# Kernel optimization log

Measured on AMD Instinct MI355X. Metric: run time of the kernel, lower is better.

The kernel has to match this reference:

```python
import jax, jax.numpy as jnp
import numpy as np

P_SIZE = 5
NUM_HEAD = 8
GN_EPS = 1e-5
LRELU_SLOPE = 0.2


def conv1x1(w, x, b=None):
    # w: [out_c, in_c], x: [n, in_c, h, w]
    y = jnp.einsum('oc,nchw->nohw', w, x)
    if b is not None:
        y = y + b[None, :, None, None]
    return y


def bilinear_sample(feat, sx, sy):
    """grid_sample(mode='bilinear', padding_mode='zeros', align_corners=True).
    With align_corners=True the normalize/denormalize round-trip in
    deformation_grid/grid_sample is the identity, so sx,sy are raw pixel coords.
    feat: [n,c,H,W]; sx,sy: [n,P,H,W] -> out [n,c,P,H,W]."""
    n, c, H, W = feat.shape
    x0 = jnp.floor(sx)
    y0 = jnp.floor(sy)
    x1 = x0 + 1.0
    y1 = y0 + 1.0
    wx1 = sx - x0
    wx0 = 1.0 - wx1
    wy1 = sy - y0
    wy0 = 1.0 - wy1
    feat_flat = feat.reshape(n, c, H * W)

    def corner(xi, yi, wgt):
        valid = (xi >= 0) & (xi <= W - 1) & (yi >= 0) & (yi <= H - 1)
        xc = jnp.clip(xi, 0, W - 1).astype(jnp.int32)
        yc = jnp.clip(yi, 0, H - 1).astype(jnp.int32)
        idx = (yc * W + xc).reshape(n, -1)                      # [n, P*H*W]
        g = jnp.take_along_axis(feat_flat, idx[:, None, :], axis=2)  # [n,c,P*H*W]
        g = g.reshape(n, c, xi.shape[1], H, W)                  # [n,c,P,H,W]
        wm = (wgt * valid.astype(feat.dtype))[:, None]          # [n,1,P,H,W]
        return g * wm

    return (corner(x0, y0, wx0 * wy0) + corner(x1, y0, wx1 * wy0)
            + corner(x0, y1, wx0 * wy1) + corner(x1, y1, wx1 * wy1))


def sample_coords(deform_field, p_size):
    # deform_field: [n,2,h,w] -> absolute pixel coords sx, sy: [n, p^2, h, w]
    n, _, h, w = deform_field.shape
    padding = (p_size - 1) // 2
    shift = jnp.arange(p_size, dtype=deform_field.dtype) - padding
    shift_y, shift_x = jnp.meshgrid(shift, shift, indexing='ij')  # [p,p]
    shift_y = shift_y.reshape(-1, 1, 1)  # [p^2,1,1]
    shift_x = shift_x.reshape(-1, 1, 1)
    gy = jnp.arange(h, dtype=deform_field.dtype)[:, None]  # [h,1]
    gx = jnp.arange(w, dtype=deform_field.dtype)[None, :]  # [1,w]
    sx = gx[None] + shift_x + deform_field[:, None, 0]     # [n,p^2,h,w]
    sy = gy[None] + shift_y + deform_field[:, None, 1]
    return sx, sy


def setup_inputs() -> dict:
    key = jax.random.key(0)
    ks = jax.random.split(key, 12)
    n, c, h, w = 2, 128, 96, 96
    hid = 256
    s = 0.05
    return {
        'query': jax.random.normal(ks[0], (n, c, h, w), jnp.float32),
        'key': jax.random.normal(ks[1], (n, c, h, w), jnp.float32),
        'value': jax.random.normal(ks[2], (n, c, h, w), jnp.float32),
        'deform_field': jax.random.normal(ks[3], (n, 2, h, w), jnp.float32) * 2.0,
        'w_q': jax.random.normal(ks[4], (c, c), jnp.float32) * s,
        'w_k': jax.random.normal(ks[5], (c, c), jnp.float32) * s,
        'w_v': jax.random.normal(ks[6], (c, c), jnp.float32) * s,
        'w_fc': jax.random.normal(ks[7], (c, c), jnp.float32) * s,
        'mlp_w1': jax.random.normal(ks[8], (hid, c), jnp.float32) * s,
        'mlp_b1': jnp.zeros((hid,), jnp.float32),
        'mlp_w2': jax.random.normal(ks[9], (c, hid), jnp.float32) * s,
        'mlp_b2': jnp.zeros((c,), jnp.float32),
        'gn_gamma': jnp.ones((c,), jnp.float32),
        'gn_beta': jnp.zeros((c,), jnp.float32),
    }


def reference(query, key, value, deform_field, w_q, w_k, w_v, w_fc,
              mlp_w1, mlp_b1, mlp_w2, mlp_b2, gn_gamma, gn_beta):
    p2 = P_SIZE * P_SIZE
    n, c, h, w = query.shape
    d_k = c // NUM_HEAD

    q = conv1x1(w_q, query)   # [n,c,h,w]
    k = conv1x1(w_k, key)
    v = conv1x1(w_v, value)

    # deformable window sampling of keys/values
    sx, sy = sample_coords(deform_field, P_SIZE)      # [n,p^2,h,w]
    k_s = bilinear_sample(k, sx, sy)                  # [n,c,p^2,h,w]
    v_s = bilinear_sample(v, sx, sy)

    # split heads
    q = q.reshape(n, NUM_HEAD, d_k, h, w)
    k_s = k_s.reshape(n, NUM_HEAD, d_k, p2, h, w)
    v_s = v_s.reshape(n, NUM_HEAD, d_k, p2, h, w)

    scale = 1.0 / jnp.sqrt(jnp.asarray(d_k, q.dtype))
    attn = jnp.einsum('nedyx,nedpyx->neyxp', q * scale, k_s)   # [n,head,h,w,p^2]
    attn = jax.nn.softmax(attn, axis=-1)
    out = jnp.einsum('neyxp,nedpyx->nedyx', attn, v_s)          # [n,head,d_v,h,w]
    out = out.reshape(n, c, h, w)
    out = conv1x1(w_fc, out)

    # conv-MLP residual
    hdn = conv1x1(mlp_w1, out, mlp_b1)
    hdn = jnp.where(hdn >= 0, hdn, LRELU_SLOPE * hdn)
    out = out + conv1x1(mlp_w2, hdn, mlp_b2)

    # GroupNorm(1, feat_dim): normalize over (C,H,W) per sample, per-channel affine
    mean = jnp.mean(out, axis=(1, 2, 3), keepdims=True)
    var = jnp.mean(jnp.square(out - mean), axis=(1, 2, 3), keepdims=True)
    out = (out - mean) * jax.lax.rsqrt(var + GN_EPS)
    out = out * gn_gamma[None, :, None, None] + gn_beta[None, :, None, None]
    return out
```

## Files before the change

### kernel.cpp

```cpp
#include <hip/hip_runtime.h>
#include <cstddef>

constexpr int Cc = 128;
constexpr int Hh = 96;
constexpr int Ww = 96;
constexpr int HW = Hh * Ww;
constexpr int Nn = 2;

typedef __attribute__((ext_vector_type(2))) _Float16 f16x2;
typedef __attribute__((ext_vector_type(4))) _Float16 f16x4;
typedef __attribute__((ext_vector_type(8))) _Float16 f16x8;
typedef __attribute__((ext_vector_type(4))) float f32x4;

__device__ __forceinline__ float fdot2(f16x2 a, f16x2 b, float c) {
#if defined(__has_builtin) && __has_builtin(__builtin_amdgcn_fdot2)
    return __builtin_amdgcn_fdot2(a, b, c, false);
#else
    return (float)a[0] * (float)b[0] + (float)a[1] * (float)b[1] + c;
#endif
}

__global__ void __launch_bounds__(256)
wcvt_k(const float* __restrict__ wq, const float* __restrict__ wk,
       const float* __restrict__ wv, const float* __restrict__ wfc,
       const float* __restrict__ w1, const float* __restrict__ w2,
       _Float16* __restrict__ dst)
{
    const int h0 = (blockIdx.x * 256 + threadIdx.x) * 8;
    const float* src; int off, K;
    if (h0 < 16384)      { src = wq;  off = h0;          K = 128; }
    else if (h0 < 32768) { src = wk;  off = h0 - 16384;  K = 128; }
    else if (h0 < 49152) { src = wv;  off = h0 - 32768;  K = 128; }
    else if (h0 < 65536) { src = wfc; off = h0 - 49152;  K = 128; }
    else if (h0 < 98304) { src = w1;  off = h0 - 65536;  K = 128; }
    else                 { src = w2;  off = h0 - 98304;  K = 256; }
    const int fid  = off >> 3;
    const int lane = fid & 63;
    const int n16  = lane & 15, quad = lane >> 4;
    const int t2   = fid >> 6;
    const int kcN  = K / 32;
    const int kc   = t2 % kcN;
    const int mt   = t2 / kcN;
    const int row  = mt * 16 + n16;
    const int col  = kc * 32 + quad * 8;
    const float* s = src + (size_t)row * K + col;
    const float4 a = *(const float4*)s;
    const float4 b = *(const float4*)(s + 4);
    f16x8 h = {(_Float16)a.x, (_Float16)a.y, (_Float16)a.z, (_Float16)a.w,
               (_Float16)b.x, (_Float16)b.y, (_Float16)b.z, (_Float16)b.w};
    *(f16x8*)&dst[h0] = h;
}

__global__ void __launch_bounds__(128)
qkv_k(const float* __restrict__ Xq, const float* __restrict__ Xk,
      const float* __restrict__ Xv, const _Float16* __restrict__ w16,
      _Float16* __restrict__ q16, _Float16* __restrict__ k16,
      _Float16* __restrict__ v16)
{
    const int t  = blockIdx.y;
    const int p0 = blockIdx.x * 64;
    const int z  = blockIdx.z;
    const float* X = (t == 0) ? Xq : (t == 1) ? Xk : Xv;
    _Float16* Y    = (t == 0) ? q16 : (t == 1) ? k16 : v16;
    const _Float16* W = w16 + (size_t)t * 16384;

    __shared__ _Float16 xl[128][72];
    const int tid = threadIdx.x;
    {
        const int px4 = (tid & 15) * 4, kg = tid >> 4;
        const float* Xz = X + (size_t)z * Cc * HW + p0 + px4;
#pragma unroll
        for (int kk = 0; kk < 16; ++kk) {
            const int k = kk * 8 + kg;
            float4 a = *(const float4*)&Xz[(size_t)k * HW];
            f16x4 h = {(_Float16)a.x, (_Float16)a.y, (_Float16)a.z, (_Float16)a.w};
            *(f16x4*)&xl[k][px4] = h;
        }
    }
    __syncthreads();

    const int w = tid >> 6, lane = tid & 63;
    const int n16 = lane & 15, quad = lane >> 4;
    const int pw = w * 32;

#pragma unroll
    for (int half = 0; half < 2; ++half) {
        const int oc0 = half * 64;
        f32x4 acc[2][4];
#pragma unroll
        for (int mi = 0; mi < 2; ++mi)
#pragma unroll
            for (int ni = 0; ni < 4; ++ni) acc[mi][ni] = (f32x4)0.f;

#pragma unroll
        for (int kcid = 0; kcid < 4; ++kcid) {
            const int kc = kcid * 32;
            f16x8 A[2], B[4];
#pragma unroll
            for (int mi = 0; mi < 2; ++mi) {
                const int px = pw + mi * 16 + n16;
                f16x8 av;
#pragma unroll
                for (int j = 0; j < 8; ++j) av[j] = xl[kc + quad * 8 + j][px];
                A[mi] = av;
            }
#pragma unroll
            for (int ni = 0; ni < 4; ++ni)
                B[ni] = *(const f16x8*)&W[(((half * 4 + ni) * 4 + kcid) * 64 + lane) * 8];
#pragma unroll
            for (int mi = 0; mi < 2; ++mi)
#pragma unroll
                for (int ni = 0; ni < 4; ++ni)
                    acc[mi][ni] = __builtin_amdgcn_mfma_f32_16x16x32_f16(
                        A[mi], B[ni], acc[mi][ni], 0, 0, 0);
        }

#pragma unroll
        for (int mi = 0; mi < 2; ++mi)
#pragma unroll
            for (int r = 0; r < 4; ++r) {
                const int pix = p0 + pw + mi * 16 + quad * 4 + r;
                const size_t base = ((size_t)z * HW + pix) * Cc + oc0;
#pragma unroll
                for (int ni = 0; ni < 4; ++ni)
                    Y[base + ni * 16 + n16] = (_Float16)acc[mi][ni][r];
            }
    }
}

template<int KT, bool OUTF16, bool BIAS, bool LRELU, bool RESID, bool REDUCE>
__global__ void __launch_bounds__(128)
mg_k(const _Float16* __restrict__ X, const _Float16* __restrict__ Wf,
     const float* __restrict__ bias, const _Float16* __restrict__ resid,
     void* __restrict__ Yv, float* __restrict__ pb, const int Mtot)
{
    constexpr int kcN = KT / 32;
    const int z = blockIdx.z, oc0 = blockIdx.y * 64, p0 = blockIdx.x * 64;
    const int tid = threadIdx.x, w = tid >> 6, lane = tid & 63;
    const int n16 = lane & 15, quad = lane >> 4;
    const _Float16* Xz = X + ((size_t)z * HW + p0 + w * 32) * KT;

    f32x4 acc[2][4];
#pragma unroll
    for (int mi = 0; mi < 2; ++mi)
#pragma unroll
        for (int ni = 0; ni < 4; ++ni) acc[mi][ni] = (f32x4)0.f;

#pragma unroll
    for (int kc = 0; kc < kcN; ++kc) {
        f16x8 A[2], B[4];
#pragma unroll
        for (int mi = 0; mi < 2; ++mi)
            A[mi] = *(const f16x8*)&Xz[(size_t)(mi * 16 + n16) * KT + kc * 32 + quad * 8];
#pragma unroll
        for (int ni = 0; ni < 4; ++ni)
            B[ni] = *(const f16x8*)&Wf[(((blockIdx.y * 4 + ni) * kcN + kc) * 64 + lane) * 8];
#pragma unroll
        for (int mi = 0; mi < 2; ++mi)
#pragma unroll
            for (int ni = 0; ni < 4; ++ni)
                acc[mi][ni] = __builtin_amdgcn_mfma_f32_16x16x32_f16(
                    A[mi], B[ni], acc[mi][ni], 0, 0, 0);
    }

    float bv[4];
#pragma unroll
    for (int ni = 0; ni < 4; ++ni) bv[ni] = BIAS ? bias[oc0 + ni * 16 + n16] : 0.f;

    float lsum = 0.f, lsq = 0.f;
#pragma unroll
    for (int mi = 0; mi < 2; ++mi)
#pragma unroll
        for (int r = 0; r < 4; ++r) {
            const int pix = p0 + w * 32 + mi * 16 + quad * 4 + r;
            const size_t ob = ((size_t)z * HW + pix) * (size_t)Mtot + oc0;
            const size_t rb = ((size_t)z * HW + pix) * 128 + oc0;
#pragma unroll
            for (int ni = 0; ni < 4; ++ni) {
                float tv = acc[mi][ni][r] + bv[ni];
                if (LRELU) tv = tv >= 0.f ? tv : 0.2f * tv;
                if (RESID) tv += (float)resid[rb + ni * 16 + n16];
                if (REDUCE) { lsum += tv; lsq += tv * tv; }
                if (OUTF16) ((_Float16*)Yv)[ob + ni * 16 + n16] = (_Float16)tv;
                else        ((float*)Yv)[ob + ni * 16 + n16] = tv;
            }
        }

    if (REDUCE) {
        __shared__ float red[4];
#pragma unroll
        for (int m = 1; m < 64; m <<= 1) {
            lsum += __shfl_xor(lsum, m, 64);
            lsq  += __shfl_xor(lsq,  m, 64);
        }
        if (lane == 0) { red[w * 2] = lsum; red[w * 2 + 1] = lsq; }
        __syncthreads();
        if (tid == 0) {
            const int bid = (blockIdx.z * gridDim.y + blockIdx.y) * gridDim.x + blockIdx.x;
            pb[bid * 2 + 0] = red[0] + red[2];
            pb[bid * 2 + 1] = red[1] + red[3];
        }
    }
}

__global__ void __launch_bounds__(256)
attn_k(const _Float16* __restrict__ q, const _Float16* __restrict__ k,
       const _Float16* __restrict__ v, const float* __restrict__ df,
       _Float16* __restrict__ out)
{
    const int blk = blockIdx.x;
    const int sw = (blk & 7) * (1152 / 8) + (blk >> 3);
    const int wv = sw * 4 + (threadIdx.x >> 6);
    const int lane = threadIdx.x & 63;
    const int gp = wv * 4 + (lane >> 4);
    const int b = gp / HW;
    const int pix = gp - b * HW;
    const int y = pix / Ww, x = pix - y * Ww;
    const int co = (lane & 15) * 8;

    const float dx = df[((size_t)b * 2 + 0) * HW + pix];
    const float dy = df[((size_t)b * 2 + 1) * HW + pix];
    const float flx = floorf(dx), fly = floorf(dy);
    const int bx = x - 2 + (int)flx;
    const int by = y - 2 + (int)fly;
    const float wx1 = dx - flx, wx0 = 1.f - wx1;
    const float wy1 = dy - fly, wy0 = 1.f - wy1;
    const float u00 = wy0 * wx0, u01 = wy0 * wx1, u10 = wy1 * wx0, u11 = wy1 * wx1;
    const float s00 = u00 * 0.25f, s01 = u01 * 0.25f,
                s10 = u10 * 0.25f, s11 = u11 * 0.25f;

    const f16x8 qv8 = *(const f16x8*)&q[((size_t)b * HW + pix) * Cc + co];
    const f16x2 q0 = {qv8[0], qv8[1]}, q1 = {qv8[2], qv8[3]},
                q2 = {qv8[4], qv8[5]}, q3 = {qv8[6], qv8[7]};

    const _Float16* kp = k + ((size_t)b * HW) * Cc + co;
    const _Float16* vp = v + ((size_t)b * HW) * Cc + co;

    const bool inb = (bx >= 0) & (by >= 0) & (bx <= Ww - 6) & (by <= Hh - 6);
    const int allin = __all(inb);

    float qk[36];
    if (allin) {
        const _Float16* kr = kp + (size_t)(by * Ww + bx) * Cc;
#pragma unroll
        for (int r = 0; r < 6; ++r) {
#pragma unroll
            for (int c = 0; c < 6; ++c) {
                const f16x8 kv = *(const f16x8*)&kr[c * Cc];
                f16x2 k0 = {kv[0], kv[1]}, k1 = {kv[2], kv[3]};
                f16x2 k2 = {kv[4], kv[5]}, k3 = {kv[6], kv[7]};
                float d = fdot2(q0, k0, 0.f);
                d = fdot2(q1, k1, d);
                d = fdot2(q2, k2, d);
                d = fdot2(q3, k3, d);
                qk[r * 6 + c] = d;
            }
            kr += Ww * Cc;
        }
    } else {
#pragma unroll
        for (int r = 0; r < 6; ++r) {
            const int yr = by + r;
            const bool rv = (yr >= 0) & (yr < Hh);
            const int yc = min(max(yr, 0), Hh - 1);
            const _Float16* kr = kp + (size_t)(yc * Ww) * Cc;
#pragma unroll
            for (int c = 0; c < 6; ++c) {
                const int xc = bx + c;
                const bool cv = rv & (xc >= 0) & (xc < Ww);
                const int xcc = min(max(xc, 0), Ww - 1);
                const f16x8 kv = *(const f16x8*)&kr[xcc * Cc];
                f16x2 k0 = {kv[0], kv[1]}, k1 = {kv[2], kv[3]};
                f16x2 k2 = {kv[4], kv[5]}, k3 = {kv[6], kv[7]};
                float d = fdot2(q0, k0, 0.f);
                d = fdot2(q1, k1, d);
                d = fdot2(q2, k2, d);
                d = fdot2(q3, k3, d);
                qk[r * 6 + c] = cv ? d : 0.f;
            }
        }
    }

    float a[25];
#pragma unroll
    for (int py = 0; py < 5; ++py)
#pragma unroll
        for (int px = 0; px < 5; ++px) {
            float tv = s00 * qk[py * 6 + px];
            tv = fmaf(s01, qk[py * 6 + px + 1], tv);
            tv = fmaf(s10, qk[(py + 1) * 6 + px], tv);
            tv = fmaf(s11, qk[(py + 1) * 6 + px + 1], tv);
            a[py * 5 + px] = tv;
        }
#pragma unroll
    for (int i = 0; i < 25; ++i) a[i] += __shfl_xor(a[i], 1, 64);

    float mx = a[0];
#pragma unroll
    for (int i = 1; i < 25; ++i) mx = fmaxf(mx, a[i]);
    float ssum = 0.f;
#pragma unroll
    for (int i = 0; i < 25; ++i) { a[i] = __expf(a[i] - mx); ssum += a[i]; }
    const float inv = 1.f / ssum;

    float tmp[6][5];
#pragma unroll
    for (int r = 0; r < 6; ++r)
#pragma unroll
        for (int px = 0; px < 5; ++px) {
            float tv = 0.f;
            if (r < 5)  tv = a[r * 5 + px] * wy0;
            if (r >= 1) tv = fmaf(a[(r - 1) * 5 + px], wy1, tv);
            tmp[r][px] = tv;
        }
    float wsum[36];
#pragma unroll
    for (int r = 0; r < 6; ++r)
#pragma unroll
        for (int c = 0; c < 6; ++c) {
            float tv = 0.f;
            if (c < 5)  tv = tmp[r][c] * wx0;
            if (c >= 1) tv = fmaf(tmp[r][c - 1], wx1, tv);
            wsum[r * 6 + c] = tv;
        }

    float o[8] = {0.f, 0.f, 0.f, 0.f, 0.f, 0.f, 0.f, 0.f};
    if (allin) {
        const _Float16* vr = vp + (size_t)(by * Ww + bx) * Cc;
#pragma unroll
        for (int r = 0; r < 6; ++r) {
#pragma unroll
            for (int c = 0; c < 6; ++c) {
                const f16x8 vv = *(const f16x8*)&vr[c * Cc];
                const float wgt = wsum[r * 6 + c];
#pragma unroll
                for (int j = 0; j < 8; ++j)
                    o[j] = fmaf(wgt, (float)vv[j], o[j]);
            }
            vr += Ww * Cc;
        }
    } else {
#pragma unroll
        for (int r = 0; r < 6; ++r) {
            const int yr = by + r;
            const bool rv = (yr >= 0) & (yr < Hh);
            const int yc = min(max(yr, 0), Hh - 1);
            const _Float16* vr = vp + (size_t)(yc * Ww) * Cc;
#pragma unroll
            for (int c = 0; c < 6; ++c) {
                const int xc = bx + c;
                const bool cv = rv & (xc >= 0) & (xc < Ww);
                const int xcc = min(max(xc, 0), Ww - 1);
                const f16x8 vv = *(const f16x8*)&vr[xcc * Cc];
                const float wgt = cv ? wsum[r * 6 + c] : 0.f;
#pragma unroll
                for (int j = 0; j < 8; ++j)
                    o[j] = fmaf(wgt, (float)vv[j], o[j]);
            }
        }
    }

    f16x8 ov;
#pragma unroll
    for (int j = 0; j < 8; ++j) ov[j] = (_Float16)(o[j] * inv);
    *(f16x8*)&out[((size_t)b * HW + pix) * Cc + co] = ov;
}

__global__ void __launch_bounds__(256)
gn_k(const float* __restrict__ y2, const float* __restrict__ pb,
     const float* __restrict__ gamma, const float* __restrict__ beta,
     float* __restrict__ out, const int nPerZ)
{
    __shared__ float t[32][68];
    __shared__ float redm[8];
    __shared__ float stats[2];
    const int z = blockIdx.z, c0 = blockIdx.y * 32, p0 = blockIdx.x * 64;
    const int tid = threadIdx.x;

    {
        float s = 0.f, qq = 0.f;
        for (int p = tid; p < nPerZ; p += 256) {
            s  += pb[(z * nPerZ + p) * 2 + 0];
            qq += pb[(z * nPerZ + p) * 2 + 1];
        }
#pragma unroll
        for (int m = 1; m < 64; m <<= 1) {
            s  += __shfl_xor(s,  m, 64);
            qq += __shfl_xor(qq, m, 64);
        }
        if ((tid & 63) == 0) {
            redm[(tid >> 6) * 2]     = s;
            redm[(tid >> 6) * 2 + 1] = qq;
        }
    }
    {
        const int px = tid >> 2, cq = tid & 3;
        const float* src = &y2[((size_t)z * HW + p0 + px) * Cc + c0 + cq * 8];
        const float4 a = *(const float4*)src;
        const float4 bq = *(const float4*)(src + 4);
        t[cq * 8 + 0][px] = a.x;  t[cq * 8 + 1][px] = a.y;
        t[cq * 8 + 2][px] = a.z;  t[cq * 8 + 3][px] = a.w;
        t[cq * 8 + 4][px] = bq.x; t[cq * 8 + 5][px] = bq.y;
        t[cq * 8 + 6][px] = bq.z; t[cq * 8 + 7][px] = bq.w;
    }
    __syncthreads();
    if (tid == 0) {
        const float invN = 1.f / (float)(Cc * HW);
        const float S = redm[0] + redm[2] + redm[4] + redm[6];
        const float Q = redm[1] + redm[3] + redm[5] + redm[7];
        const float mean = S * invN;
        const float var  = fmaf(-mean, mean, Q * invN);
        stats[0] = mean;
        stats[1] = rsqrtf(var + 1e-5f);
    }
    __syncthreads();
    {
        const float mean = stats[0], rs = stats[1];
        const int c = tid >> 3, pq = tid & 7;
        const float g = gamma[c0 + c] * rs, be = beta[c0 + c];
        float4 o1, o2;
        o1.x = fmaf(t[c][pq * 8 + 0] - mean, g, be);
        o1.y = fmaf(t[c][pq * 8 + 1] - mean, g, be);
        o1.z = fmaf(t[c][pq * 8 + 2] - mean, g, be);
        o1.w = fmaf(t[c][pq * 8 + 3] - mean, g, be);
        o2.x = fmaf(t[c][pq * 8 + 4] - mean, g, be);
        o2.y = fmaf(t[c][pq * 8 + 5] - mean, g, be);
        o2.z = fmaf(t[c][pq * 8 + 6] - mean, g, be);
        o2.w = fmaf(t[c][pq * 8 + 7] - mean, g, be);
        float* dst = &out[((size_t)z * Cc + c0 + c) * HW + p0 + pq * 8];
        *(float4*)dst = o1;
        *(float4*)(dst + 4) = o2;
    }
}

extern "C" void kernel_launch(void* const* d_in, const int* in_sizes, int n_in,
                              void* d_out, int out_size, void* d_ws, size_t ws_size,
                              hipStream_t stream)
{
    const float* query  = (const float*)d_in[0];
    const float* key    = (const float*)d_in[1];
    const float* value  = (const float*)d_in[2];
    const float* deform = (const float*)d_in[3];
    const float* w_q    = (const float*)d_in[4];
    const float* w_k    = (const float*)d_in[5];
    const float* w_v    = (const float*)d_in[6];
    const float* w_fc   = (const float*)d_in[7];
    const float* mlp_w1 = (const float*)d_in[8];
    const float* mlp_b1 = (const float*)d_in[9];
    const float* mlp_w2 = (const float*)d_in[10];
    const float* mlp_b2 = (const float*)d_in[11];
    const float* gn_g   = (const float*)d_in[12];
    const float* gn_b   = (const float*)d_in[13];
    float* out = (float*)d_out;

    char* wsb = (char*)d_ws;
    _Float16* w16 = (_Float16*)wsb;
    float* pb   = (float*)(wsb + 262144);
    _Float16* T = (_Float16*)(wsb + 524288);
    const size_t S16 = (size_t)Nn * HW * Cc;
    _Float16* q16  = T;
    _Float16* k16  = T + S16;
    _Float16* v16  = T + 2 * S16;
    _Float16* at16 = T + 3 * S16;
    _Float16* y1   = T + 4 * S16;
    _Float16* hb   = T;
    float*    y2   = (float*)(T + 2 * S16);

    wcvt_k<<<dim3(64), dim3(256), 0, stream>>>(
        w_q, w_k, w_v, w_fc, mlp_w1, mlp_w2, w16);

    qkv_k<<<dim3(HW / 64, 3, Nn), dim3(128), 0, stream>>>(
        query, key, value, w16, q16, k16, v16);

    attn_k<<<dim3(Nn * HW / 16), dim3(256), 0, stream>>>(
        q16, k16, v16, deform, at16);

    mg_k<128, true, false, false, false, false>
        <<<dim3(HW / 64, 2, Nn), dim3(128), 0, stream>>>(
        at16, w16 + 49152, nullptr, nullptr, y1, nullptr, 128);

    mg_k<128, true, true, true, false, false>
        <<<dim3(HW / 64, 4, Nn), dim3(128), 0, stream>>>(
        y1, w16 + 65536, mlp_b1, nullptr, hb, nullptr, 256);

    mg_k<256, false, true, false, true, true>
        <<<dim3(HW / 64, 2, Nn), dim3(128), 0, stream>>>(
        hb, w16 + 98304, mlp_b2, y1, y2, pb, 128);

    gn_k<<<dim3(HW / 64, Cc / 32, Nn), dim3(256), 0, stream>>>(
        y2, pb, gn_g, gn_b, out, 288);
}
```

Before: 156.8 us.

## Fuse fc, MLP up/down projections into one kernel with LDS intermediates

Measured after the change: 176.7 us. 12.7% more time.

```diff
diff --git a/kernel.cpp b/kernel.cpp
--- a/kernel.cpp
+++ b/kernel.cpp
@@ -128,81 +128,6 @@
     }
 }
 
-template<int KT, bool OUTF16, bool BIAS, bool LRELU, bool RESID, bool REDUCE>
-__global__ void __launch_bounds__(128)
-mg_k(const _Float16* __restrict__ X, const _Float16* __restrict__ Wf,
-     const float* __restrict__ bias, const _Float16* __restrict__ resid,
-     void* __restrict__ Yv, float* __restrict__ pb, const int Mtot)
-{
-    constexpr int kcN = KT / 32;
-    const int z = blockIdx.z, oc0 = blockIdx.y * 64, p0 = blockIdx.x * 64;
-    const int tid = threadIdx.x, w = tid >> 6, lane = tid & 63;
-    const int n16 = lane & 15, quad = lane >> 4;
-    const _Float16* Xz = X + ((size_t)z * HW + p0 + w * 32) * KT;
-
-    f32x4 acc[2][4];
-#pragma unroll
-    for (int mi = 0; mi < 2; ++mi)
-#pragma unroll
-        for (int ni = 0; ni < 4; ++ni) acc[mi][ni] = (f32x4)0.f;
-
-#pragma unroll
-    for (int kc = 0; kc < kcN; ++kc) {
-        f16x8 A[2], B[4];
-#pragma unroll
-        for (int mi = 0; mi < 2; ++mi)
-            A[mi] = *(const f16x8*)&Xz[(size_t)(mi * 16 + n16) * KT + kc * 32 + quad * 8];
-#pragma unroll
-        for (int ni = 0; ni < 4; ++ni)
-            B[ni] = *(const f16x8*)&Wf[(((blockIdx.y * 4 + ni) * kcN + kc) * 64 + lane) * 8];
-#pragma unroll
-        for (int mi = 0; mi < 2; ++mi)
-#pragma unroll
-            for (int ni = 0; ni < 4; ++ni)
-                acc[mi][ni] = __builtin_amdgcn_mfma_f32_16x16x32_f16(
-                    A[mi], B[ni], acc[mi][ni], 0, 0, 0);
-    }
-
-    float bv[4];
-#pragma unroll
-    for (int ni = 0; ni < 4; ++ni) bv[ni] = BIAS ? bias[oc0 + ni * 16 + n16] : 0.f;
-
-    float lsum = 0.f, lsq = 0.f;
-#pragma unroll
-    for (int mi = 0; mi < 2; ++mi)
-#pragma unroll
-        for (int r = 0; r < 4; ++r) {
-            const int pix = p0 + w * 32 + mi * 16 + quad * 4 + r;
-            const size_t ob = ((size_t)z * HW + pix) * (size_t)Mtot + oc0;
-            const size_t rb = ((size_t)z * HW + pix) * 128 + oc0;
-#pragma unroll
-            for (int ni = 0; ni < 4; ++ni) {
-                float tv = acc[mi][ni][r] + bv[ni];
-                if (LRELU) tv = tv >= 0.f ? tv : 0.2f * tv;
-                if (RESID) tv += (float)resid[rb + ni * 16 + n16];
-                if (REDUCE) { lsum += tv; lsq += tv * tv; }
-                if (OUTF16) ((_Float16*)Yv)[ob + ni * 16 + n16] = (_Float16)tv;
-                else        ((float*)Yv)[ob + ni * 16 + n16] = tv;
-            }
-        }
-
-    if (REDUCE) {
-        __shared__ float red[4];
-#pragma unroll
-        for (int m = 1; m < 64; m <<= 1) {
-            lsum += __shfl_xor(lsum, m, 64);
-            lsq  += __shfl_xor(lsq,  m, 64);
-        }
-        if (lane == 0) { red[w * 2] = lsum; red[w * 2 + 1] = lsq; }
-        __syncthreads();
-        if (tid == 0) {
-            const int bid = (blockIdx.z * gridDim.y + blockIdx.y) * gridDim.x + blockIdx.x;
-            pb[bid * 2 + 0] = red[0] + red[2];
-            pb[bid * 2 + 1] = red[1] + red[3];
-        }
-    }
-}
-
 __global__ void __launch_bounds__(256)
 attn_k(const _Float16* __restrict__ q, const _Float16* __restrict__ k,
        const _Float16* __restrict__ v, const float* __restrict__ df,
@@ -366,8 +291,106 @@
     *(f16x8*)&out[((size_t)b * HW + pix) * Cc + co] = ov;
 }
 
+__global__ void __launch_bounds__(128)
+mlp_k(const _Float16* __restrict__ at, const _Float16* __restrict__ wfc,
+      const _Float16* __restrict__ w1, const _Float16* __restrict__ w2,
+      const float* __restrict__ b1, const float* __restrict__ b2,
+      _Float16* __restrict__ y2, float* __restrict__ pb)
+{
+    __shared__ _Float16 y1l[32][138];
+    __shared__ _Float16 hl[32][276];
+
+    const int z = blockIdx.y, p0 = blockIdx.x * 32;
+    const int tid = threadIdx.x, w = tid >> 6, lane = tid & 63;
+    const int n16 = lane & 15, quad = lane >> 4;
+    const int pw = w * 16;
+
+    {
+        const _Float16* Az = at + ((size_t)z * HW + p0 + pw) * 128;
+        f32x4 acc[8];
+#pragma unroll
+        for (int ni = 0; ni < 8; ++ni) acc[ni] = (f32x4)0.f;
+#pragma unroll
+        for (int kc = 0; kc < 4; ++kc) {
+            const f16x8 A = *(const f16x8*)&Az[(size_t)n16 * 128 + kc * 32 + quad * 8];
+#pragma unroll
+            for (int ni = 0; ni < 8; ++ni) {
+                const f16x8 B = *(const f16x8*)&wfc[((ni * 4 + kc) * 64 + lane) * 8];
+                acc[ni] = __builtin_amdgcn_mfma_f32_16x16x32_f16(A, B, acc[ni], 0, 0, 0);
+            }
+        }
+#pragma unroll
+        for (int ni = 0; ni < 8; ++ni)
+#pragma unroll
+            for (int r = 0; r < 4; ++r)
+                y1l[pw + quad * 4 + r][ni * 16 + n16] = (_Float16)acc[ni][r];
+    }
+
+    {
+        f32x4 acc[16];
+#pragma unroll
+        for (int ni = 0; ni < 16; ++ni) acc[ni] = (f32x4)0.f;
+#pragma unroll
+        for (int kc = 0; kc < 4; ++kc) {
+            const f16x8 A = *(const f16x8*)&y1l[pw + n16][kc * 32 + quad * 8];
+#pragma unroll
+            for (int ni = 0; ni < 16; ++ni) {
+                const f16x8 B = *(const f16x8*)&w1[((ni * 4 + kc) * 64 + lane) * 8];
+                acc[ni] = __builtin_amdgcn_mfma_f32_16x16x32_f16(A, B, acc[ni], 0, 0, 0);
+            }
+        }
+#pragma unroll
+        for (int ni = 0; ni < 16; ++ni) {
+            const float bv = b1[ni * 16 + n16];
+#pragma unroll
+            for (int r = 0; r < 4; ++r) {
+                float t = acc[ni][r] + bv;
+                t = t >= 0.f ? t : 0.2f * t;
+                hl[pw + quad * 4 + r][ni * 16 + n16] = (_Float16)t;
+            }
+        }
+    }
+
+    {
+        f32x4 acc[8];
+#pragma unroll
+        for (int ni = 0; ni < 8; ++ni) acc[ni] = (f32x4)0.f;
+#pragma unroll
+        for (int kc = 0; kc < 8; ++kc) {
+            const f16x8 A = *(const f16x8*)&hl[pw + n16][kc * 32 + quad * 8];
+#pragma unroll
+            for (int ni = 0; ni < 8; ++ni) {
+                const f16x8 B = *(const f16x8*)&w2[((ni * 8 + kc) * 64 + lane) * 8];
+                acc[ni] = __builtin_amdgcn_mfma_f32_16x16x32_f16(A, B, acc[ni], 0, 0, 0);
+            }
+        }
+        float lsum = 0.f, lsq = 0.f;
+#pragma unroll
+        for (int ni = 0; ni < 8; ++ni) {
+            const float bv = b2[ni * 16 + n16];
+#pragma unroll
+            for (int r = 0; r < 4; ++r) {
+                const int px = pw + quad * 4 + r;
+                float t = acc[ni][r] + bv + (float)y1l[px][ni * 16 + n16];
+                lsum += t; lsq += t * t;
+                y2[((size_t)z * HW + p0 + px) * 128 + ni * 16 + n16] = (_Float16)t;
+            }
+        }
+#pragma unroll
+        for (int m = 1; m < 64; m <<= 1) {
+            lsum += __shfl_xor(lsum, m, 64);
+            lsq  += __shfl_xor(lsq,  m, 64);
+        }
+        if (lane == 0) {
+            const int bid = (z * gridDim.x + blockIdx.x) * 2 + w;
+            pb[bid * 2 + 0] = lsum;
+            pb[bid * 2 + 1] = lsq;
+        }
+    }
+}
+
 __global__ void __launch_bounds__(256)
-gn_k(const float* __restrict__ y2, const float* __restrict__ pb,
+gn_k(const _Float16* __restrict__ y2, const float* __restrict__ pb,
      const float* __restrict__ gamma, const float* __restrict__ beta,
      float* __restrict__ out, const int nPerZ)
 {
@@ -395,13 +418,9 @@
     }
     {
         const int px = tid >> 2, cq = tid & 3;
-        const float* src = &y2[((size_t)z * HW + p0 + px) * Cc + c0 + cq * 8];
-        const float4 a = *(const float4*)src;
-        const float4 bq = *(const float4*)(src + 4);
-        t[cq * 8 + 0][px] = a.x;  t[cq * 8 + 1][px] = a.y;
-        t[cq * 8 + 2][px] = a.z;  t[cq * 8 + 3][px] = a.w;
-        t[cq * 8 + 4][px] = bq.x; t[cq * 8 + 5][px] = bq.y;
-        t[cq * 8 + 6][px] = bq.z; t[cq * 8 + 7][px] = bq.w;
+        const f16x8 vv = *(const f16x8*)&y2[((size_t)z * HW + p0 + px) * Cc + c0 + cq * 8];
+#pragma unroll
+        for (int j = 0; j < 8; ++j) t[cq * 8 + j][px] = (float)vv[j];
     }
     __syncthreads();
     if (tid == 0) {
@@ -462,9 +481,7 @@
     _Float16* k16  = T + S16;
     _Float16* v16  = T + 2 * S16;
     _Float16* at16 = T + 3 * S16;
-    _Float16* y1   = T + 4 * S16;
-    _Float16* hb   = T;
-    float*    y2   = (float*)(T + 2 * S16);
+    _Float16* y2   = T + 4 * S16;
 
     wcvt_k<<<dim3(64), dim3(256), 0, stream>>>(
         w_q, w_k, w_v, w_fc, mlp_w1, mlp_w2, w16);
@@ -475,18 +492,10 @@
     attn_k<<<dim3(Nn * HW / 16), dim3(256), 0, stream>>>(
         q16, k16, v16, deform, at16);
 
-    mg_k<128, true, false, false, false, false>
-        <<<dim3(HW / 64, 2, Nn), dim3(128), 0, stream>>>(
-        at16, w16 + 49152, nullptr, nullptr, y1, nullptr, 128);
-
-    mg_k<128, true, true, true, false, false>
-        <<<dim3(HW / 64, 4, Nn), dim3(128), 0, stream>>>(
-        y1, w16 + 65536, mlp_b1, nullptr, hb, nullptr, 256);
-
-    mg_k<256, false, true, false, true, true>
-        <<<dim3(HW / 64, 2, Nn), dim3(128), 0, stream>>>(
-        hb, w16 + 98304, mlp_b2, y1, y2, pb, 128);
+    mlp_k<<<dim3(HW / 32, Nn), dim3(128), 0, stream>>>(
+        at16, w16 + 49152, w16 + 65536, w16 + 98304,
+        mlp_b1, mlp_b2, y2, pb);
 
     gn_k<<<dim3(HW / 64, Cc / 32, Nn), dim3(256), 0, stream>>>(
-        y2, pb, gn_g, gn_b, out, 288);
-}
+        y2, pb, gn_g, gn_b, out, (HW / 32) * 2);
+}
```
